# Kernel tuning notes

Measured on AMD Instinct MI355X. Metric: run time of the kernel, lower is better.

The kernel has to match this reference:

```python
import jax, jax.numpy as jnp
import numpy as np

B, C, FRAMES, E, W = 8, 2, 3999, 512, 16
STEP = W // 2  # frame_step = W//2 = 8


def setup_inputs() -> dict:
    key = jax.random.key(0)
    k1, k2 = jax.random.split(key)
    dec_input = jax.random.normal(k1, (B, C, FRAMES, E), dtype=jnp.float32)
    weight = jax.random.normal(k2, (W, E), dtype=jnp.float32) * (1.0 / np.sqrt(E))
    return {"dec_input": dec_input, "weight": weight}


def overlap_and_add(signal, frame_step):
    # signal: [..., frames, frame_length] -> [..., (frames-1)*step + frame_length]
    frames, frame_length = signal.shape[-2], signal.shape[-1]
    output_size = frame_step * (frames - 1) + frame_length
    # target sample index of every element of `signal`
    idx = (jnp.arange(frames)[:, None] * frame_step
           + jnp.arange(frame_length)[None, :]).reshape(-1)  # [frames*frame_length]
    flat = signal.reshape(*signal.shape[:-2], frames * frame_length)
    out = jnp.zeros((*signal.shape[:-2], output_size), dtype=signal.dtype)
    # scatter-accumulate overlapping frames along the last axis
    return out.at[..., idx].add(flat)


def reference(dec_input, weight):
    # dec_input: [B, C, frames, E]; weight: [W, E] (nn.Linear(E, W, bias=False))
    est_source = jnp.einsum('bcle,we->bclw', dec_input, weight)  # [B, C, frames, W]
    return overlap_and_add(est_source, STEP)  # [B, C, T]
```

## Files before the change

kernel.cpp:

```cpp
#include <hip/hip_runtime.h>
#include <cstdint>
#include <cstddef>


#define NBC     16
#define FRAMES  3999
#define EE      512
#define TOUT    32000
#define NGROUP  4000
#define GPB     63

__global__ __launch_bounds__(256, 4) void decoder_kernel(
    const float* __restrict__ dec,
    const float* __restrict__ wgt,
    float* __restrict__ out)
{
    __shared__ float red[4 * 16 * 64];

    const int tid   = threadIdx.x;
    const int bc    = blockIdx.x >> 6;
    const int chunk = blockIdx.x & 63;
    const int g0    = chunk * GPB;

    const int s = tid & 63;
    const int q = __builtin_amdgcn_readfirstlane(tid >> 6);

    const int f = g0 - 1 + s;
    const float vmask = (f >= 0 && f < FRAMES) ? 1.0f : 0.0f;
    const int fr = min(max(f, 0), FRAMES - 1);

    const float* arow  = dec + ((size_t)bc * FRAMES + fr) * EE + q * 128;
    const float* wrow  = wgt + q * 128;

    float acc[16];
    #pragma unroll
    for (int w = 0; w < 16; ++w) acc[w] = 0.f;

    float4 xv[2][4];
    #pragma unroll
    for (int u = 0; u < 4; ++u)
        xv[0][u] = *(const float4*)(arow + 4 * u);

    #pragma unroll
    for (int c = 0; c < 8; ++c) {
        const int cur = c & 1;
        if (c < 7) {
            #pragma unroll
            for (int u = 0; u < 4; ++u)
                xv[cur ^ 1][u] = *(const float4*)(arow + (c + 1) * 16 + 4 * u);
        }
        #pragma unroll
        for (int w = 0; w < 16; ++w) {
            const float* wr = wrow + w * EE + c * 16;
            float sum = acc[w];
            #pragma unroll
            for (int u = 0; u < 4; ++u) {
                sum += xv[cur][u].x * wr[4 * u + 0];
                sum += xv[cur][u].y * wr[4 * u + 1];
                sum += xv[cur][u].z * wr[4 * u + 2];
                sum += xv[cur][u].w * wr[4 * u + 3];
            }
            acc[w] = sum;
        }
    }

    #pragma unroll
    for (int w = 0; w < 16; ++w)
        red[(q * 16 + w) * 64 + s] = acc[w] * vmask;
    __syncthreads();

    for (int o = tid; o < GPB * 8; o += 256) {
        const int j = o >> 3;
        const int i = o & 7;
        const int g = g0 + j;
        if (g < NGROUP) {
            float v = 0.f;
            #pragma unroll
            for (int qq = 0; qq < 4; ++qq)
                v += red[(qq * 16 + i) * 64 + (j + 1)]
                   + red[(qq * 16 + 8 + i) * 64 + j];
            out[(size_t)bc * TOUT + g * 8 + i] = v;
        }
    }
}

extern "C" void kernel_launch(void* const* d_in, const int* in_sizes, int n_in,
                              void* d_out, int out_size, void* d_ws, size_t ws_size,
                              hipStream_t stream) {
    const float* dec = (const float*)d_in[0];
    const float* wgt = (const float*)d_in[1];
    float* out = (float*)d_out;

    decoder_kernel<<<dim3(1024), dim3(256), 0, stream>>>(dec, wgt, out);
}
```

Measured before the change: 200.6 us.

## Stage input rows in LDS via async global-to-LDS loads and split outputs across waves

Instead of each wave reading a quarter of the embedding dimension into registers and reducing across waves, the block now stages 64-column tiles of the input frames into double-buffered shared memory using direct global-to-LDS loads with an XOR swizzle. Each wave computes the full dot product for four of the sixteen output columns, which removes the cross-wave reduction in the epilogue. This adds a block barrier per tile and LDS read traffic, and each wave re-reads all input data from LDS.

```diff
diff --git a/kernel.cpp b/kernel.cpp
--- a/kernel.cpp
+++ b/kernel.cpp
@@ -10,77 +10,102 @@
 #define NGROUP  4000
 #define GPB     63
 
+__device__ __forceinline__ void gload_lds16(const float* src, float* dst) {
+    __builtin_amdgcn_global_load_lds(
+        (const __attribute__((address_space(1))) void*)src,
+        (__attribute__((address_space(3))) void*)dst,
+        16, 0, 0);
+}
+
 __global__ __launch_bounds__(256, 4) void decoder_kernel(
     const float* __restrict__ dec,
     const float* __restrict__ wgt,
     float* __restrict__ out)
 {
-    __shared__ float red[4 * 16 * 64];
+    __shared__ __align__(16) float xbuf[2][64 * 64];
+    float* red = xbuf[0];
 
     const int tid   = threadIdx.x;
     const int bc    = blockIdx.x >> 6;
     const int chunk = blockIdx.x & 63;
     const int g0    = chunk * GPB;
 
-    const int s = tid & 63;
-    const int q = __builtin_amdgcn_readfirstlane(tid >> 6);
+    const int s    = tid & 63;
+    const int lane = tid & 63;
+    const int h    = __builtin_amdgcn_readfirstlane(tid >> 6);
 
     const int f = g0 - 1 + s;
     const float vmask = (f >= 0 && f < FRAMES) ? 1.0f : 0.0f;
-    const int fr = min(max(f, 0), FRAMES - 1);
 
-    const float* arow  = dec + ((size_t)bc * FRAMES + fr) * EE + q * 128;
-    const float* wrow  = wgt + q * 128;
+    const float* decb = dec + (size_t)bc * FRAMES * EE;
 
-    float acc[16];
+    const float* srcp[4];
+    float*       dstp[4];
     #pragma unroll
-    for (int w = 0; w < 16; ++w) acc[w] = 0.f;
+    for (int i = 0; i < 4; ++i) {
+        const int l  = h * 256 + i * 64 + lane;
+        const int fs = l >> 4;
+        const int us = (l & 15) ^ (fs & 7);
+        const int ff = min(max(g0 - 1 + fs, 0), FRAMES - 1);
+        srcp[i] = decb + (size_t)ff * EE + us * 4;
+        dstp[i] = &xbuf[0][0] + (size_t)l * 4;
+    }
 
-    float4 xv[2][4];
+    float acc[4] = {0.f, 0.f, 0.f, 0.f};
+    const float* wb = wgt + (h * 4) * EE;
+
     #pragma unroll
-    for (int u = 0; u < 4; ++u)
-        xv[0][u] = *(const float4*)(arow + 4 * u);
+    for (int i = 0; i < 4; ++i)
+        gload_lds16(srcp[i], dstp[i]);
+    __syncthreads();
 
     #pragma unroll
     for (int c = 0; c < 8; ++c) {
         const int cur = c & 1;
         if (c < 7) {
+            const int nxt = (c + 1) & 1;
             #pragma unroll
-            for (int u = 0; u < 4; ++u)
-                xv[cur ^ 1][u] = *(const float4*)(arow + (c + 1) * 16 + 4 * u);
+            for (int i = 0; i < 4; ++i)
+                gload_lds16(srcp[i] + (c + 1) * 64, dstp[i] + nxt * 4096);
         }
+
+        const float* xb = xbuf[cur];
         #pragma unroll
-        for (int w = 0; w < 16; ++w) {
-            const float* wr = wrow + w * EE + c * 16;
-            float sum = acc[w];
+        for (int hf = 0; hf < 2; ++hf) {
+            float4 xv[8];
             #pragma unroll
-            for (int u = 0; u < 4; ++u) {
-                sum += xv[cur][u].x * wr[4 * u + 0];
-                sum += xv[cur][u].y * wr[4 * u + 1];
-                sum += xv[cur][u].z * wr[4 * u + 2];
-                sum += xv[cur][u].w * wr[4 * u + 3];
+            for (int u8 = 0; u8 < 8; ++u8) {
+                const int u = hf * 8 + u8;
+                xv[u8] = *(const float4*)(xb + s * 64 + ((4 * u) ^ ((s & 7) << 2)));
             }
-            acc[w] = sum;
+            #pragma unroll
+            for (int w = 0; w < 4; ++w) {
+                const float* wr = wb + w * EE + c * 64 + hf * 32;
+                #pragma unroll
+                for (int u8 = 0; u8 < 8; ++u8) {
+                    acc[w] += xv[u8].x * wr[4 * u8 + 0]
+                            + xv[u8].y * wr[4 * u8 + 1]
+                            + xv[u8].z * wr[4 * u8 + 2]
+                            + xv[u8].w * wr[4 * u8 + 3];
+                }
+            }
         }
+        __syncthreads();
     }
 
     #pragma unroll
-    for (int w = 0; w < 16; ++w)
-        red[(q * 16 + w) * 64 + s] = acc[w] * vmask;
+    for (int w = 0; w < 4; ++w)
+        red[(h * 4 + w) * 64 + s] = acc[w] * vmask;
     __syncthreads();
 
     for (int o = tid; o < GPB * 8; o += 256) {
         const int j = o >> 3;
         const int i = o & 7;
         const int g = g0 + j;
-        if (g < NGROUP) {
-            float v = 0.f;
-            #pragma unroll
-            for (int qq = 0; qq < 4; ++qq)
-                v += red[(qq * 16 + i) * 64 + (j + 1)]
-                   + red[(qq * 16 + 8 + i) * 64 + j];
-            out[(size_t)bc * TOUT + g * 8 + i] = v;
-        }
+        if (g < NGROUP)
+            out[(size_t)bc * TOUT + g * 8 + i]
+                = red[i * 64 + (j + 1)]
+                + red[(8 + i) * 64 + j];
     }
 }
 
```

Measured after the change: 216.0 us. 1.08x slower.

## Stage frame rows through per-wave LDS double buffer with coalesced global loads

Applied to the files above, without the earlier changes.

Global loads are reorganised so four adjacent lanes cooperatively read a 64-byte row segment. Each instruction then covers 16 frames, instead of every lane fetching its own strided row. The data is written into a padded per-wave LDS double buffer and read back as float4 per lane for the FMA loop. The reduction buffer stride is also padded to 65 to avoid LDS bank conflicts. The cost is extra LDS traffic and an added barrier, and correctness relies on same-wave LDS ordering without a barrier inside the loop.

```diff
diff --git a/kernel.cpp b/kernel.cpp
--- a/kernel.cpp
+++ b/kernel.cpp
@@ -9,64 +9,92 @@
 #define TOUT    32000
 #define NGROUP  4000
 #define GPB     63
+#define RSTR    65
+#define XSTR    20
+#define BUFSTEP (64 * XSTR)
 
 __global__ __launch_bounds__(256, 4) void decoder_kernel(
     const float* __restrict__ dec,
     const float* __restrict__ wgt,
     float* __restrict__ out)
 {
-    __shared__ float red[4 * 16 * 64];
+    __shared__ __align__(16) float xs[4 * 2 * BUFSTEP];
+    float* red = xs;
 
     const int tid   = threadIdx.x;
     const int bc    = blockIdx.x >> 6;
     const int chunk = blockIdx.x & 63;
     const int g0    = chunk * GPB;
 
-    const int s = tid & 63;
-    const int q = __builtin_amdgcn_readfirstlane(tid >> 6);
+    const int lane = tid & 63;
+    const int s    = lane;
+    const int q    = __builtin_amdgcn_readfirstlane(tid >> 6);
 
     const int f = g0 - 1 + s;
     const float vmask = (f >= 0 && f < FRAMES) ? 1.0f : 0.0f;
-    const int fr = min(max(f, 0), FRAMES - 1);
 
-    const float* arow  = dec + ((size_t)bc * FRAMES + fr) * EE + q * 128;
-    const float* wrow  = wgt + q * 128;
+    const float* decb = dec + (size_t)bc * FRAMES * EE;
+
+    const float* sp[4];
+    int          dp[4];
+    #pragma unroll
+    for (int i = 0; i < 4; ++i) {
+        const int fi = i * 16 + (lane >> 2);
+        const int j  = lane & 3;
+        const int fr = min(max(g0 - 1 + fi, 0), FRAMES - 1);
+        sp[i] = decb + (size_t)fr * EE + q * 128 + j * 4;
+        dp[i] = (q * 2) * BUFSTEP + fi * XSTR + j * 4;
+    }
+    const int xrb = (q * 2) * BUFSTEP + s * XSTR;
+
+    const float* wq = wgt + q * 128;
 
     float acc[16];
     #pragma unroll
     for (int w = 0; w < 16; ++w) acc[w] = 0.f;
 
-    float4 xv[2][4];
-    #pragma unroll
-    for (int u = 0; u < 4; ++u)
-        xv[0][u] = *(const float4*)(arow + 4 * u);
+    {
+        float4 t[4];
+        #pragma unroll
+        for (int i = 0; i < 4; ++i) t[i] = *(const float4*)(sp[i]);
+        #pragma unroll
+        for (int i = 0; i < 4; ++i) *(float4*)(xs + dp[i]) = t[i];
+    }
 
     #pragma unroll
     for (int c = 0; c < 8; ++c) {
         const int cur = c & 1;
+        const int nxt = cur ^ 1;
+
+        float4 xg[4];
         if (c < 7) {
             #pragma unroll
-            for (int u = 0; u < 4; ++u)
-                xv[cur ^ 1][u] = *(const float4*)(arow + (c + 1) * 16 + 4 * u);
+            for (int i = 0; i < 4; ++i)
+                xg[i] = *(const float4*)(sp[i] + (c + 1) * 16);
         }
+
         #pragma unroll
-        for (int w = 0; w < 16; ++w) {
-            const float* wr = wrow + w * EE + c * 16;
-            float sum = acc[w];
+        for (int u = 0; u < 4; ++u) {
+            const float4 xv = *(const float4*)(xs + xrb + cur * BUFSTEP + u * 4);
             #pragma unroll
-            for (int u = 0; u < 4; ++u) {
-                sum += xv[cur][u].x * wr[4 * u + 0];
-                sum += xv[cur][u].y * wr[4 * u + 1];
-                sum += xv[cur][u].z * wr[4 * u + 2];
-                sum += xv[cur][u].w * wr[4 * u + 3];
+            for (int w = 0; w < 16; ++w) {
+                const float* wr = wq + w * EE + c * 16 + u * 4;
+                acc[w] += xv.x * wr[0] + xv.y * wr[1]
+                        + xv.z * wr[2] + xv.w * wr[3];
             }
-            acc[w] = sum;
+        }
+
+        if (c < 7) {
+            #pragma unroll
+            for (int i = 0; i < 4; ++i)
+                *(float4*)(xs + dp[i] + nxt * BUFSTEP) = xg[i];
         }
     }
 
+    __syncthreads();
     #pragma unroll
     for (int w = 0; w < 16; ++w)
-        red[(q * 16 + w) * 64 + s] = acc[w] * vmask;
+        red[(q * 16 + w) * RSTR + s] = acc[w] * vmask;
     __syncthreads();
 
     for (int o = tid; o < GPB * 8; o += 256) {
@@ -77,8 +105,8 @@
             float v = 0.f;
             #pragma unroll
             for (int qq = 0; qq < 4; ++qq)
-                v += red[(qq * 16 + i) * 64 + (j + 1)]
-                   + red[(qq * 16 + 8 + i) * 64 + j];
+                v += red[(qq * 16 + i) * RSTR + (j + 1)]
+                   + red[(qq * 16 + 8 + i) * RSTR + j];
             out[(size_t)bc * TOUT + g * 8 + i] = v;
         }
     }
```

Result: no change. 200.9 us (+0.1%).
